# Kernel optimization log

Hardware: AMD Instinct MI355X
Metric: run time of the kernel (lower is better)

Reference implementation:

```python
import jax, jax.numpy as jnp
import numpy as np

N_NODES = 50000
N_EDGES = 1250000
D_IN = 256
D_OUT = 64


def setup_inputs() -> dict:
    key = jax.random.key(0)
    k0, k1, k2, k3, k4 = jax.random.split(key, 5)
    return {
        "arg0_1": jax.random.normal(k0, (D_OUT, D_IN), dtype=jnp.float32),
        "arg1_1": jax.random.normal(k1, (D_OUT,), dtype=jnp.float32),
        "arg2_1": jax.random.randint(k2, (2, N_EDGES), 0, N_NODES, dtype=jnp.int64),
        "arg3_1": jax.random.uniform(k3, (N_EDGES,), dtype=jnp.float32),
        "arg4_1": jax.random.normal(k4, (N_NODES, D_IN), dtype=jnp.float32),
    }


def reference(arg0_1, arg1_1, arg2_1, arg3_1, arg4_1):
    # h = x @ W^T  : [N, D_OUT]
    h = jnp.matmul(arg4_1, arg0_1.T)
    src = arg2_1[0]  # gather indices
    dst = arg2_1[1]  # scatter_add indices
    # edge messages: gather source rows, scale by edge weight  : [E, D_OUT]
    msg = arg3_1[:, None] * h[src]
    # scatter_add into node buckets
    agg = jax.ops.segment_sum(msg, dst, num_segments=N_NODES)
    return agg + arg1_1
```

## Files before the change

### kernel.cpp

```cpp
#include <hip/hip_runtime.h>
#include <hip/hip_bf16.h>

#define D_IN    256
#define D_OUT   64
#define NNODES  50000
#define NEDGES  1250000

#define BUCK_SHIFT 8
#define BUCK_NODES 256
#define NBUCK      196
#define CPAD       16
#define EPB        4096
#define NB_EDGE    ((NEDGES + EPB - 1) / EPB)
#define BCAP    8128

typedef float f32x4 __attribute__((ext_vector_type(4)));
typedef short s16x8 __attribute__((ext_vector_type(8)));

static __device__ __forceinline__ unsigned short f2bf(float f) {
    union { float f; unsigned u; } v; v.f = f;
    unsigned r = v.u + 0x7FFFu + ((v.u >> 16) & 1u);
    return (unsigned short)(r >> 16);
}

__global__ __launch_bounds__(256) void gemm_h_mfma(
    const float* __restrict__ x, const float* __restrict__ W,
    signed char* __restrict__ hq, float* __restrict__ scale_tab, int N)
{
    __shared__ uint4 sW[2048];

    const int t    = threadIdx.x;
    const int lane = t & 63;
    const int wave = t >> 6;
    const int m    = lane & 15;
    const int q    = lane >> 4;

    #pragma unroll
    for (int i = 0; i < 8; ++i) {
        int slot = t + i * 256;
        int ln   = slot & 63;
        int kb   = (slot >> 6) & 7;
        int c    = slot >> 9;
        int lm = ln & 15, lq = ln >> 4;
        const float* wp = W + (c * 16 + lm) * D_IN + kb * 32 + lq * 8;
        float4 w0 = *(const float4*)wp;
        float4 w1 = *(const float4*)(wp + 4);
        uint4 u;
        u.x = (unsigned)f2bf(w0.x) | ((unsigned)f2bf(w0.y) << 16);
        u.y = (unsigned)f2bf(w0.z) | ((unsigned)f2bf(w0.w) << 16);
        u.z = (unsigned)f2bf(w1.x) | ((unsigned)f2bf(w1.y) << 16);
        u.w = (unsigned)f2bf(w1.z) | ((unsigned)f2bf(w1.w) << 16);
        sW[slot] = u;
    }
    __syncthreads();

    const int rowA = blockIdx.x * 64 + wave * 16 + m;
    const int rowc = (rowA < N) ? rowA : (N - 1);
    const float* xr = x + (long long)rowc * D_IN + q * 8;

    f32x4 acc[4] = {};

    #pragma unroll
    for (int kb = 0; kb < 8; ++kb) {
        float4 a0 = *(const float4*)(xr + kb * 32);
        float4 a1 = *(const float4*)(xr + kb * 32 + 4);
        s16x8 af;
        af[0] = (short)f2bf(a0.x); af[1] = (short)f2bf(a0.y);
        af[2] = (short)f2bf(a0.z); af[3] = (short)f2bf(a0.w);
        af[4] = (short)f2bf(a1.x); af[5] = (short)f2bf(a1.y);
        af[6] = (short)f2bf(a1.z); af[7] = (short)f2bf(a1.w);

        #pragma unroll
        for (int c = 0; c < 4; ++c) {
            s16x8 bf = *(const s16x8*)&sW[(c * 8 + kb) * 64 + lane];
            acc[c] = __builtin_amdgcn_mfma_f32_16x16x32_bf16(af, bf, acc[c], 0, 0, 0);
        }
    }

    #pragma unroll
    for (int r = 0; r < 4; ++r) {
        float local = fmaxf(fmaxf(fabsf(acc[0][r]), fabsf(acc[1][r])),
                            fmaxf(fabsf(acc[2][r]), fabsf(acc[3][r])));
        #pragma unroll
        for (int msk = 1; msk < 16; msk <<= 1)
            local = fmaxf(local, __shfl_xor(local, msk));
        float amax = fmaxf(local, 1e-6f);
        float inv  = 127.0f / amax;
        int gr = blockIdx.x * 64 + wave * 16 + q * 4 + r;
        if (gr < N) {
            if (m == 0) scale_tab[gr] = amax * (1.0f / 127.0f);
            #pragma unroll
            for (int c = 0; c < 4; ++c) {
                int qv = __float2int_rn(acc[c][r] * inv);
                hq[(long long)gr * D_OUT + c * 16 + m] = (signed char)qv;
            }
        }
    }
}

__global__ __launch_bounds__(256) void bin_edges(
    const int* __restrict__ src, const int* __restrict__ dst,
    const float* __restrict__ wt, const float* __restrict__ scale_tab,
    int* __restrict__ bcursor, unsigned long long* __restrict__ binned)
{
    __shared__ int lcnt[NBUCK];
    __shared__ int lbase[NBUCK];
    int t = threadIdx.x;

    for (int i = t; i < NBUCK; i += 256) lcnt[i] = 0;
    __syncthreads();

    int base = blockIdx.x * EPB;
    bool full = (base + EPB <= NEDGES);

    if (full) {
        const int4* d4 = (const int4*)(dst + base);
        #pragma unroll
        for (int it = 0; it < 4; ++it) {
            int4 d = d4[t + it * 256];
            atomicAdd(&lcnt[d.x >> BUCK_SHIFT], 1);
            atomicAdd(&lcnt[d.y >> BUCK_SHIFT], 1);
            atomicAdd(&lcnt[d.z >> BUCK_SHIFT], 1);
            atomicAdd(&lcnt[d.w >> BUCK_SHIFT], 1);
        }
    } else {
        for (int e = base + t; e < NEDGES; e += 256)
            atomicAdd(&lcnt[dst[e] >> BUCK_SHIFT], 1);
    }
    __syncthreads();

    if (t < NBUCK) {
        int c = lcnt[t];
        lbase[t] = c ? (t * BCAP + atomicAdd(&bcursor[t * CPAD], c)) : 0;
        lcnt[t]  = 0;
    }
    __syncthreads();

    if (full) {
        const int4*   s4 = (const int4*)(src + base);
        const int4*   d4 = (const int4*)(dst + base);
        const float4* w4 = (const float4*)(wt + base);
        #pragma unroll
        for (int it = 0; it < 4; ++it) {
            int4   ss = s4[t + it * 256];
            int4   dd = d4[t + it * 256];
            float4 ww = w4[t + it * 256];
            int sv[4]   = {ss.x, ss.y, ss.z, ss.w};
            int dv[4]   = {dd.x, dd.y, dd.z, dd.w};
            float wv[4] = {ww.x, ww.y, ww.z, ww.w};
            #pragma unroll
            for (int k = 0; k < 4; ++k) {
                int d = dv[k];
                int b = d >> BUCK_SHIFT;
                int r = atomicAdd(&lcnt[b], 1);
                float wf = wv[k] * scale_tab[sv[k]];
                unsigned lo = (unsigned)sv[k] | ((unsigned)(d & (BUCK_NODES - 1)) << 16);
                unsigned long long rec = (unsigned long long)lo
                                       | ((unsigned long long)__float_as_uint(wf) << 32);
                binned[lbase[b] + r] = rec;
            }
        }
    } else {
        for (int e = base + t; e < NEDGES; e += 256) {
            int d = dst[e];
            int b = d >> BUCK_SHIFT;
            int r = atomicAdd(&lcnt[b], 1);
            int sidx = src[e];
            float wf = wt[e] * scale_tab[sidx];
            unsigned lo = (unsigned)sidx | ((unsigned)(d & (BUCK_NODES - 1)) << 16);
            unsigned long long rec = (unsigned long long)lo
                                   | ((unsigned long long)__float_as_uint(wf) << 32);
            binned[lbase[b] + r] = rec;
        }
    }
}

__global__ __launch_bounds__(512) void sort_buckets(
    const unsigned long long* __restrict__ binned, const int* __restrict__ bcursor,
    unsigned long long* __restrict__ csr,
    int* __restrict__ starts, int* __restrict__ counts)
{
    __shared__ int s[256];
    __shared__ int lcnt[BUCK_NODES];
    __shared__ int lcur[BUCK_NODES];
    __shared__ int sh_s0, sh_cnt;
    int t = threadIdx.x;
    int b = blockIdx.x;

    int v = 0;
    if (t < 256) {
        v = (t < NBUCK) ? bcursor[t * CPAD] : 0;
        s[t] = v;
        lcnt[t] = 0;
    }
    __syncthreads();
    #pragma unroll
    for (int off = 1; off < 256; off <<= 1) {
        int u = (t < 256 && t >= off) ? s[t - off] : 0;
        __syncthreads();
        if (t < 256) s[t] += u;
        __syncthreads();
    }
    if (t == b) { sh_s0 = s[t] - v; sh_cnt = v; }
    __syncthreads();
    int s0 = sh_s0, cntb = sh_cnt;
    int node0 = b << BUCK_SHIFT;
    int nn = min(BUCK_NODES, NNODES - node0);
    const unsigned long long* bsrc = binned + (long long)b * BCAP;

    for (int k = t; k < cntb; k += 512)
        atomicAdd(&lcnt[(int)((bsrc[k] >> 16) & 0xFF)], 1);
    __syncthreads();

    int v2 = 0;
    if (t < 256) { v2 = lcnt[t]; s[t] = v2; }
    __syncthreads();
    #pragma unroll
    for (int off = 1; off < 256; off <<= 1) {
        int u = (t < 256 && t >= off) ? s[t - off] : 0;
        __syncthreads();
        if (t < 256) s[t] += u;
        __syncthreads();
    }
    if (t < 256) {
        int excl = s[t] - v2;
        lcur[t] = s0 + excl;
        if (t < nn) {
            starts[node0 + t] = s0 + excl;
            counts[node0 + t] = v2;
        }
    }
    __syncthreads();

    for (int k = t; k < cntb; k += 512) {
        unsigned long long r = bsrc[k];
        int dloc = (int)((r >> 16) & 0xFF);
        int pos  = atomicAdd(&lcur[dloc], 1);
        csr[pos] = r;
    }
}

__global__ __launch_bounds__(256) void agg_nodes(
    const int2* __restrict__ recs, const int* __restrict__ starts,
    const int* __restrict__ counts, const signed char* __restrict__ hq,
    const float* __restrict__ bias, float* __restrict__ out)
{
    int wid  = (blockIdx.x * 256 + threadIdx.x) >> 6;
    int node = __builtin_amdgcn_readfirstlane(wid);
    if (node >= NNODES) return;
    int lane = threadIdx.x & 63;

    float acc = bias[lane];
    int s0  = starts[node];
    int cnt = counts[node];
    int i = s0, e = s0 + cnt;

    for (; i + 7 < e; i += 8) {
        int2 r0 = recs[i + 0];
        int2 r1 = recs[i + 1];
        int2 r2 = recs[i + 2];
        int2 r3 = recs[i + 3];
        int2 r4 = recs[i + 4];
        int2 r5 = recs[i + 5];
        int2 r6 = recs[i + 6];
        int2 r7 = recs[i + 7];
        float v0 = (float)hq[(r0.x & 0xFFFF) * D_OUT + lane];
        float v1 = (float)hq[(r1.x & 0xFFFF) * D_OUT + lane];
        float v2 = (float)hq[(r2.x & 0xFFFF) * D_OUT + lane];
        float v3 = (float)hq[(r3.x & 0xFFFF) * D_OUT + lane];
        float v4 = (float)hq[(r4.x & 0xFFFF) * D_OUT + lane];
        float v5 = (float)hq[(r5.x & 0xFFFF) * D_OUT + lane];
        float v6 = (float)hq[(r6.x & 0xFFFF) * D_OUT + lane];
        float v7 = (float)hq[(r7.x & 0xFFFF) * D_OUT + lane];
        acc += __int_as_float(r0.y) * v0;
        acc += __int_as_float(r1.y) * v1;
        acc += __int_as_float(r2.y) * v2;
        acc += __int_as_float(r3.y) * v3;
        acc += __int_as_float(r4.y) * v4;
        acc += __int_as_float(r5.y) * v5;
        acc += __int_as_float(r6.y) * v6;
        acc += __int_as_float(r7.y) * v7;
    }
    for (; i + 3 < e; i += 4) {
        int2 r0 = recs[i + 0];
        int2 r1 = recs[i + 1];
        int2 r2 = recs[i + 2];
        int2 r3 = recs[i + 3];
        float v0 = (float)hq[(r0.x & 0xFFFF) * D_OUT + lane];
        float v1 = (float)hq[(r1.x & 0xFFFF) * D_OUT + lane];
        float v2 = (float)hq[(r2.x & 0xFFFF) * D_OUT + lane];
        float v3 = (float)hq[(r3.x & 0xFFFF) * D_OUT + lane];
        acc += __int_as_float(r0.y) * v0;
        acc += __int_as_float(r1.y) * v1;
        acc += __int_as_float(r2.y) * v2;
        acc += __int_as_float(r3.y) * v3;
    }
    for (; i < e; ++i) {
        int2 r = recs[i];
        acc += __int_as_float(r.y) * (float)hq[(r.x & 0xFFFF) * D_OUT + lane];
    }
    out[(long long)node * D_OUT + lane] = acc;
}

__global__ __launch_bounds__(256) void init_bias(
    float* __restrict__ out, const float* __restrict__ bias, int total)
{
    int i = blockIdx.x * blockDim.x + threadIdx.x;
    if (i < total) out[i] = bias[i & (D_OUT - 1)];
}

__global__ __launch_bounds__(256) void scatter_edges(
    const int* __restrict__ src, const int* __restrict__ dst,
    const float* __restrict__ wt, const signed char* __restrict__ hq,
    const float* __restrict__ scale_tab, float* __restrict__ out)
{
    long long gid = (long long)blockIdx.x * blockDim.x + threadIdx.x;
    int e    = (int)(gid >> 6);
    int lane = threadIdx.x & 63;
    if (e < NEDGES) {
        int   s = src[e];
        int   d = dst[e];
        float w = wt[e] * scale_tab[s];
        float v = w * (float)hq[(long long)s * D_OUT + lane];
        atomicAdd(&out[(long long)d * D_OUT + lane], v);
    }
}

extern "C" void kernel_launch(void* const* d_in, const int* in_sizes, int n_in,
                              void* d_out, int out_size, void* d_ws, size_t ws_size,
                              hipStream_t stream)
{
    const float* W     = (const float*)d_in[0];
    const float* bias  = (const float*)d_in[1];
    const int*   edges = (const int*)  d_in[2];
    const float* wt    = (const float*)d_in[3];
    const float* x     = (const float*)d_in[4];
    float*       out   = (float*)d_out;

    const int* src = edges;
    const int* dst = edges + NEDGES;

    char* ws = (char*)d_ws;
    const size_t OFF_HQ     = 0;
    const size_t OFF_SCALE  = 3200000;
    const size_t OFF_RECS   = 3400000;
    const size_t OFF_STARTS = 13400000;
    const size_t OFF_COUNTS = 13600000;
    const size_t OFF_BCUR   = 13800000;
    const size_t REQUIRED   = 13812544;

    signed char* hq        = (signed char*)(ws + OFF_HQ);
    float*       scale_tab = (float*)(ws + OFF_SCALE);

    if (ws_size >= REQUIRED) {
        unsigned long long* csr     = (unsigned long long*)(ws + OFF_RECS);
        int*                starts  = (int*)(ws + OFF_STARTS);
        int*                counts  = (int*)(ws + OFF_COUNTS);
        int*                bcursor = (int*)(ws + OFF_BCUR);

        unsigned long long* binned = (unsigned long long*)d_out;

        hipMemsetAsync(bcursor, 0, NBUCK * CPAD * sizeof(int), stream);

        gemm_h_mfma<<<(NNODES + 63) / 64, 256, 0, stream>>>(
            x, W, hq, scale_tab, NNODES);

        bin_edges<<<NB_EDGE, 256, 0, stream>>>(src, dst, wt, scale_tab,
                                               bcursor, binned);

        sort_buckets<<<NBUCK, 512, 0, stream>>>(binned, bcursor, csr,
                                                starts, counts);

        int nb = (NNODES * 64 + 255) / 256;
        agg_nodes<<<nb, 256, 0, stream>>>((const int2*)csr, starts, counts,
                                          hq, bias, out);
    } else {
        gemm_h_mfma<<<(NNODES + 63) / 64, 256, 0, stream>>>(
            x, W, hq, scale_tab, NNODES);
        int total = NNODES * D_OUT;
        init_bias<<<(total + 255) / 256, 256, 0, stream>>>(out, bias, total);
        long long threads = (long long)NEDGES * 64;
        int blocks = (int)((threads + 255) / 256);
        scatter_edges<<<blocks, 256, 0, stream>>>(src, dst, wt, hq, scale_tab, out);
    }
}
```

Before: 184.2 us.

## Fuse GEMM and edge binning into one launch, move scale multiply to sort

Merges the quantizing GEMM and the edge-binning pass into one kernel whose extra blocks bin edges, so both independent stages run concurrently in a single launch. Binning no longer depends on scale_tab, so the per-edge scale multiply moves into sort_buckets, which runs after the GEMM has finished. This removes one launch and the serialization between GEMM and binning. In exchange, the fused kernel carries the GEMM's shared-memory footprint into the binning blocks, which may lower their occupancy.

```diff
diff --git a/kernel.cpp b/kernel.cpp
--- a/kernel.cpp
+++ b/kernel.cpp
@@ -12,6 +12,7 @@
 #define CPAD       16
 #define EPB        4096
 #define NB_EDGE    ((NEDGES + EPB - 1) / EPB)
+#define GEMM_BLOCKS ((NNODES + 63) / 64)
 #define BCAP    8128
 
 typedef float f32x4 __attribute__((ext_vector_type(4)));
@@ -23,13 +24,87 @@
     return (unsigned short)(r >> 16);
 }
 
-__global__ __launch_bounds__(256) void gemm_h_mfma(
+__global__ __launch_bounds__(256) void gemm_bin(
     const float* __restrict__ x, const float* __restrict__ W,
-    signed char* __restrict__ hq, float* __restrict__ scale_tab, int N)
+    signed char* __restrict__ hq, float* __restrict__ scale_tab, int N,
+    const int* __restrict__ src, const int* __restrict__ dst,
+    const float* __restrict__ wt,
+    int* __restrict__ bcursor, unsigned long long* __restrict__ binned)
 {
     __shared__ uint4 sW[2048];
-
-    const int t    = threadIdx.x;
+    __shared__ int   lcnt[NBUCK];
+    __shared__ int   lbase[NBUCK];
+
+    const int t = threadIdx.x;
+
+    if (blockIdx.x >= GEMM_BLOCKS) {
+        for (int i = t; i < NBUCK; i += 256) lcnt[i] = 0;
+        __syncthreads();
+
+        int base = (blockIdx.x - GEMM_BLOCKS) * EPB;
+        bool full = (base + EPB <= NEDGES);
+
+        if (full) {
+            const int4* d4 = (const int4*)(dst + base);
+            #pragma unroll
+            for (int it = 0; it < 4; ++it) {
+                int4 d = d4[t + it * 256];
+                atomicAdd(&lcnt[d.x >> BUCK_SHIFT], 1);
+                atomicAdd(&lcnt[d.y >> BUCK_SHIFT], 1);
+                atomicAdd(&lcnt[d.z >> BUCK_SHIFT], 1);
+                atomicAdd(&lcnt[d.w >> BUCK_SHIFT], 1);
+            }
+        } else {
+            for (int e = base + t; e < NEDGES; e += 256)
+                atomicAdd(&lcnt[dst[e] >> BUCK_SHIFT], 1);
+        }
+        __syncthreads();
+
+        if (t < NBUCK) {
+            int c = lcnt[t];
+            lbase[t] = c ? (t * BCAP + atomicAdd(&bcursor[t * CPAD], c)) : 0;
+            lcnt[t]  = 0;
+        }
+        __syncthreads();
+
+        if (full) {
+            const int4*   s4 = (const int4*)(src + base);
+            const int4*   d4 = (const int4*)(dst + base);
+            const float4* w4 = (const float4*)(wt + base);
+            #pragma unroll
+            for (int it = 0; it < 4; ++it) {
+                int4   ss = s4[t + it * 256];
+                int4   dd = d4[t + it * 256];
+                float4 ww = w4[t + it * 256];
+                int sv[4]   = {ss.x, ss.y, ss.z, ss.w};
+                int dv[4]   = {dd.x, dd.y, dd.z, dd.w};
+                float wv[4] = {ww.x, ww.y, ww.z, ww.w};
+                #pragma unroll
+                for (int k = 0; k < 4; ++k) {
+                    int d = dv[k];
+                    int b = d >> BUCK_SHIFT;
+                    int r = atomicAdd(&lcnt[b], 1);
+                    unsigned lo = (unsigned)sv[k] | ((unsigned)(d & (BUCK_NODES - 1)) << 16);
+                    unsigned long long rec = (unsigned long long)lo
+                                           | ((unsigned long long)__float_as_uint(wv[k]) << 32);
+                    binned[lbase[b] + r] = rec;
+                }
+            }
+        } else {
+            for (int e = base + t; e < NEDGES; e += 256) {
+                int d = dst[e];
+                int b = d >> BUCK_SHIFT;
+                int r = atomicAdd(&lcnt[b], 1);
+                int sidx = src[e];
+                unsigned lo = (unsigned)sidx | ((unsigned)(d & (BUCK_NODES - 1)) << 16);
+                unsigned long long rec = (unsigned long long)lo
+                                       | ((unsigned long long)__float_as_uint(wt[e]) << 32);
+                binned[lbase[b] + r] = rec;
+            }
+        }
+        return;
+    }
+
     const int lane = t & 63;
     const int wave = t >> 6;
     const int m    = lane & 15;
@@ -98,85 +173,9 @@
     }
 }
 
-__global__ __launch_bounds__(256) void bin_edges(
-    const int* __restrict__ src, const int* __restrict__ dst,
-    const float* __restrict__ wt, const float* __restrict__ scale_tab,
-    int* __restrict__ bcursor, unsigned long long* __restrict__ binned)
-{
-    __shared__ int lcnt[NBUCK];
-    __shared__ int lbase[NBUCK];
-    int t = threadIdx.x;
-
-    for (int i = t; i < NBUCK; i += 256) lcnt[i] = 0;
-    __syncthreads();
-
-    int base = blockIdx.x * EPB;
-    bool full = (base + EPB <= NEDGES);
-
-    if (full) {
-        const int4* d4 = (const int4*)(dst + base);
-        #pragma unroll
-        for (int it = 0; it < 4; ++it) {
-            int4 d = d4[t + it * 256];
-            atomicAdd(&lcnt[d.x >> BUCK_SHIFT], 1);
-            atomicAdd(&lcnt[d.y >> BUCK_SHIFT], 1);
-            atomicAdd(&lcnt[d.z >> BUCK_SHIFT], 1);
-            atomicAdd(&lcnt[d.w >> BUCK_SHIFT], 1);
-        }
-    } else {
-        for (int e = base + t; e < NEDGES; e += 256)
-            atomicAdd(&lcnt[dst[e] >> BUCK_SHIFT], 1);
-    }
-    __syncthreads();
-
-    if (t < NBUCK) {
-        int c = lcnt[t];
-        lbase[t] = c ? (t * BCAP + atomicAdd(&bcursor[t * CPAD], c)) : 0;
-        lcnt[t]  = 0;
-    }
-    __syncthreads();
-
-    if (full) {
-        const int4*   s4 = (const int4*)(src + base);
-        const int4*   d4 = (const int4*)(dst + base);
-        const float4* w4 = (const float4*)(wt + base);
-        #pragma unroll
-        for (int it = 0; it < 4; ++it) {
-            int4   ss = s4[t + it * 256];
-            int4   dd = d4[t + it * 256];
-            float4 ww = w4[t + it * 256];
-            int sv[4]   = {ss.x, ss.y, ss.z, ss.w};
-            int dv[4]   = {dd.x, dd.y, dd.z, dd.w};
-            float wv[4] = {ww.x, ww.y, ww.z, ww.w};
-            #pragma unroll
-            for (int k = 0; k < 4; ++k) {
-                int d = dv[k];
-                int b = d >> BUCK_SHIFT;
-                int r = atomicAdd(&lcnt[b], 1);
-                float wf = wv[k] * scale_tab[sv[k]];
-                unsigned lo = (unsigned)sv[k] | ((unsigned)(d & (BUCK_NODES - 1)) << 16);
-                unsigned long long rec = (unsigned long long)lo
-                                       | ((unsigned long long)__float_as_uint(wf) << 32);
-                binned[lbase[b] + r] = rec;
-            }
-        }
-    } else {
-        for (int e = base + t; e < NEDGES; e += 256) {
-            int d = dst[e];
-            int b = d >> BUCK_SHIFT;
-            int r = atomicAdd(&lcnt[b], 1);
-            int sidx = src[e];
-            float wf = wt[e] * scale_tab[sidx];
-            unsigned lo = (unsigned)sidx | ((unsigned)(d & (BUCK_NODES - 1)) << 16);
-            unsigned long long rec = (unsigned long long)lo
-                                   | ((unsigned long long)__float_as_uint(wf) << 32);
-            binned[lbase[b] + r] = rec;
-        }
-    }
-}
-
 __global__ __launch_bounds__(512) void sort_buckets(
     const unsigned long long* __restrict__ binned, const int* __restrict__ bcursor,
+    const float* __restrict__ scale_tab,
     unsigned long long* __restrict__ csr,
     int* __restrict__ starts, int* __restrict__ counts)
 {
@@ -235,8 +234,11 @@
     for (int k = t; k < cntb; k += 512) {
         unsigned long long r = bsrc[k];
         int dloc = (int)((r >> 16) & 0xFF);
+        int sidx = (int)(r & 0xFFFF);
+        float wf = __uint_as_float((unsigned)(r >> 32)) * scale_tab[sidx];
         int pos  = atomicAdd(&lcur[dloc], 1);
-        csr[pos] = r;
+        csr[pos] = (r & 0xFFFFFFFFull)
+                 | ((unsigned long long)__float_as_uint(wf) << 32);
     }
 }
 
@@ -362,21 +364,20 @@
 
         hipMemsetAsync(bcursor, 0, NBUCK * CPAD * sizeof(int), stream);
 
-        gemm_h_mfma<<<(NNODES + 63) / 64, 256, 0, stream>>>(
-            x, W, hq, scale_tab, NNODES);
-
-        bin_edges<<<NB_EDGE, 256, 0, stream>>>(src, dst, wt, scale_tab,
-                                               bcursor, binned);
-
-        sort_buckets<<<NBUCK, 512, 0, stream>>>(binned, bcursor, csr,
-                                                starts, counts);
+        gemm_bin<<<GEMM_BLOCKS + NB_EDGE, 256, 0, stream>>>(
+            x, W, hq, scale_tab, NNODES, src, dst, wt, bcursor, binned);
+
+        sort_buckets<<<NBUCK, 512, 0, stream>>>(binned, bcursor, scale_tab,
+                                                csr, starts, counts);
 
         int nb = (NNODES * 64 + 255) / 256;
         agg_nodes<<<nb, 256, 0, stream>>>((const int2*)csr, starts, counts,
                                           hq, bias, out);
     } else {
-        gemm_h_mfma<<<(NNODES + 63) / 64, 256, 0, stream>>>(
-            x, W, hq, scale_tab, NNODES);
+        gemm_bin<<<GEMM_BLOCKS, 256, 0, stream>>>(
+            x, W, hq, scale_tab, NNODES,
+            (const int*)nullptr, (const int*)nullptr, (const float*)nullptr,
+            (int*)nullptr, (unsigned long long*)nullptr);
         int total = NNODES * D_OUT;
         init_bias<<<(total + 255) / 256, 256, 0, stream>>>(out, bias, total);
         long long threads = (long long)NEDGES * 64;
```

After: 170.0 us. 1.08x faster.
